# Kernel optimization log

Measured on AMD Instinct MI355X. Metric: run time of the kernel, lower is better.

Reference implementation:

```python
import jax, jax.numpy as jnp
import numpy as np

N = 50000
E = 800000
D_IN = 128
D_HID = 128
NUM_LAYERS = 3


def setup_inputs() -> dict:
    key = jax.random.key(0)
    ks = jax.random.split(key, 8)
    x = jax.random.normal(ks[0], (N, D_IN), dtype=jnp.float32)
    edge_index = jax.random.randint(ks[1], (2, E), 0, N, dtype=jnp.int64)
    edge_weight = jnp.ones((E,), dtype=jnp.float32)
    # GCNConv params: glorot-ish weights [in, out], zero bias
    def w(k, fi, fo):
        return jax.random.normal(k, (fi, fo), dtype=jnp.float32) * (1.0 / np.sqrt(fi))
    W0 = w(ks[2], D_IN, D_HID)
    b0 = jnp.zeros((D_HID,), dtype=jnp.float32)
    W1 = w(ks[3], D_HID, D_HID)
    b1 = jnp.zeros((D_HID,), dtype=jnp.float32)
    W2 = w(ks[4], D_HID, D_HID)
    b2 = jnp.zeros((D_HID,), dtype=jnp.float32)
    return {"x": x, "edge_index": edge_index, "edge_weight": edge_weight,
            "W0": W0, "b0": b0, "W1": W1, "b1": b1, "W2": W2, "b2": b2}


def _gcn_layer(h, src, dst, norm, W, b, n):
    # linear transform then degree-normalized scatter-add aggregation
    h = h @ W                                   # [N, d_out]
    msg = h[src] * norm[:, None]                # gather + scale, [E+N, d_out]
    out = jax.ops.segment_sum(msg, dst, num_segments=n)  # scatter-add
    return out + b


def reference(x, edge_index, edge_weight, W0, b0, W1, b1, W2, b2):
    n = x.shape[0]
    loop = jnp.arange(n, dtype=edge_index.dtype)
    src = jnp.concatenate([edge_index[0], loop])   # add self-loops (fill=1)
    dst = jnp.concatenate([edge_index[1], loop])
    ew = jnp.concatenate([edge_weight, jnp.ones((n,), dtype=edge_weight.dtype)])
    # symmetric normalization: deg computed on target (col), norm = d^-1/2[src]*w*d^-1/2[dst]
    deg = jax.ops.segment_sum(ew, dst, num_segments=n)
    dis = jnp.where(deg > 0, jax.lax.rsqrt(deg), 0.0)
    norm = dis[src] * ew * dis[dst]               # [E+N]
    z = x
    for (W, b) in ((W0, b0), (W1, b1), (W2, b2)):
        z = _gcn_layer(z, src, dst, norm, W, b, n)
        z = jax.nn.relu(z)
    return z
```

## Files before the change

kernel.cpp:

```cpp
#include <hip/hip_runtime.h>

#define D 128
#define NB 250
#define BN 200
#define NBLK 512
#define CAP 7168

typedef float f2v __attribute__((ext_vector_type(2)));
typedef short bf16x8 __attribute__((ext_vector_type(8)));
typedef float f32x4 __attribute__((ext_vector_type(4)));

__device__ __forceinline__ unsigned bf16r(float f) {
  unsigned u = __float_as_uint(f);
  return (u + 0x7fffu + ((u >> 16) & 1u)) >> 16;
}


__global__ __launch_bounds__(256) void k_pre1(const int* __restrict__ dst, int* __restrict__ M, int E,
                                              const float* __restrict__ X, unsigned short* __restrict__ Xb,
                                              int total4, int GC,
                                              const float* __restrict__ W0, const float* __restrict__ W1,
                                              const float* __restrict__ W2, unsigned short* __restrict__ Wt) {
  __shared__ int lh[NB];
  int b = blockIdx.x;
  int tid = threadIdx.x;
  if (b < NBLK) {
    for (int i = tid; i < NB; i += 256) lh[i] = 0;
    __syncthreads();
    const int EPB = (E + NBLK - 1) / NBLK;
    int e0 = b * EPB;
    int e1 = min(e0 + EPB, E);
    for (int e = e0 + tid; e < e1; e += 256) atomicAdd(&lh[dst[e] / BN], 1);
    __syncthreads();
    for (int i = tid; i < NB; i += 256) M[i * NBLK + b] = lh[i];
  } else if (b < NBLK + GC) {
    int i = (b - NBLK) * 256 + tid;
    if (i < total4) {
      float4 v = ((const float4*)X)[i];
      ushort4 o;
      o.x = (unsigned short)bf16r(v.x);
      o.y = (unsigned short)bf16r(v.y);
      o.z = (unsigned short)bf16r(v.z);
      o.w = (unsigned short)bf16r(v.w);
      ((ushort4*)Xb)[i] = o;
    }
  } else {
    int i = (b - NBLK - GC) * 256 + tid;
    if (i < 3 * 16384) {
      int l = i >> 14;
      int r = i & 16383;
      int nn = r >> 7, kk = r & 127;
      const float* W = (l == 0) ? W0 : (l == 1) ? W1 : W2;
      Wt[i] = (unsigned short)bf16r(W[kk * 128 + nn]);
    }
  }
}


__global__ __launch_bounds__(256) void k_blocksum(const int* __restrict__ cnt, int* __restrict__ bsum, int n) {
  int i = blockIdx.x * 256 + threadIdx.x;
  int v = (i < n) ? cnt[i] : 0;
#pragma unroll
  for (int off = 32; off > 0; off >>= 1) v += __shfl_down(v, off);
  __shared__ int ws[4];
  if ((threadIdx.x & 63) == 0) ws[threadIdx.x >> 6] = v;
  __syncthreads();
  if (threadIdx.x == 0) bsum[blockIdx.x] = ws[0] + ws[1] + ws[2] + ws[3];
}

__global__ __launch_bounds__(512) void k_scanb2(const int* __restrict__ bsum, int* __restrict__ boff, int nb) {
  __shared__ int s[512];
  int t = threadIdx.x;
  int v = (t < nb) ? bsum[t] : 0;
  s[t] = v;
  __syncthreads();
#pragma unroll
  for (int off = 1; off < 512; off <<= 1) {
    int u = (t >= off) ? s[t - off] : 0;
    __syncthreads();
    s[t] += u;
    __syncthreads();
  }
  if (t < nb) boff[t] = s[t] - v;
}

__global__ __launch_bounds__(256) void k_scanm(int* __restrict__ M, const int* __restrict__ boff,
                                               int* __restrict__ bbase, int flatN, int Etot) {
  __shared__ int s[256];
  int t = threadIdx.x;
  int i = blockIdx.x * 256 + t;
  int v = (i < flatN) ? M[i] : 0;
  s[t] = v;
  __syncthreads();
#pragma unroll
  for (int off = 1; off < 256; off <<= 1) {
    int u = (t >= off) ? s[t - off] : 0;
    __syncthreads();
    s[t] += u;
    __syncthreads();
  }
  int ex = s[t] - v + boff[blockIdx.x];
  if (i < flatN) {
    M[i] = ex;
    if ((i & (NBLK - 1)) == 0) bbase[i / NBLK] = ex;
  }
  if (i == 0) bbase[NB] = Etot;
}


__global__ __launch_bounds__(256) void k_pre2(const unsigned short* __restrict__ Zb,
                                              const unsigned short* __restrict__ Wt,
                                              unsigned short* __restrict__ H, int n, int GG,
                                              const int* __restrict__ src, const int* __restrict__ dst,
                                              const float* __restrict__ ew, const int* __restrict__ M,
                                              uint2* __restrict__ part, int E) {
  __shared__ int lcur[NB];
  int b = blockIdx.x;
  if (b < GG) {
    int lane = threadIdx.x & 63;
    int wid  = threadIdx.x >> 6;
    int row0 = b * 16;
    int r  = lane & 15;
    int kg = lane >> 4;
    int c0 = wid * 32;
    const size_t abase  = (size_t)(row0 + r) * 128 + kg * 8;
    const size_t b0base = (size_t)(c0 + r) * 128 + kg * 8;
    const size_t b1base = (size_t)(c0 + 16 + r) * 128 + kg * 8;
    f32x4 acc0 = {0.f, 0.f, 0.f, 0.f};
    f32x4 acc1 = {0.f, 0.f, 0.f, 0.f};
#pragma unroll
    for (int k0 = 0; k0 < 128; k0 += 32) {
      bf16x8 a  = *(const bf16x8*)&Zb[abase + k0];
      bf16x8 b0 = *(const bf16x8*)&Wt[b0base + k0];
      bf16x8 b1 = *(const bf16x8*)&Wt[b1base + k0];
      acc0 = __builtin_amdgcn_mfma_f32_16x16x32_bf16(a, b0, acc0, 0, 0, 0);
      acc1 = __builtin_amdgcn_mfma_f32_16x16x32_bf16(a, b1, acc1, 0, 0, 0);
    }
    int orow = row0 + kg * 4;
#pragma unroll
    for (int j = 0; j < 4; ++j) {
      H[(size_t)(orow + j) * 128 + c0 + r]      = (unsigned short)bf16r(acc0[j]);
      H[(size_t)(orow + j) * 128 + c0 + 16 + r] = (unsigned short)bf16r(acc1[j]);
    }
  } else {
    int blk = b - GG;
    int tid = threadIdx.x;
    for (int i = tid; i < NB; i += 256) lcur[i] = M[i * NBLK + blk];
    __syncthreads();
    const int EPB = (E + NBLK - 1) / NBLK;
    int e0 = blk * EPB;
    int e1 = min(e0 + EPB, E);
    for (int e = e0 + tid; e < e1; e += 256) {
      int d = dst[e];
      int bkt = d / BN;
      int dlow = d - bkt * BN;
      int p = atomicAdd(&lcur[bkt], 1);
      uint2 rec;
      rec.x = (unsigned)src[e] | ((unsigned)dlow << 24);
      rec.y = __float_as_uint(ew[e]);
      part[p] = rec;
    }
  }
}


__global__ __launch_bounds__(256) void k_bsort(const uint2* __restrict__ part, const int* __restrict__ bbase,
                                               uint2* __restrict__ csr, int* __restrict__ rowptr,
                                               float* __restrict__ dis, int n, int E) {
  __shared__ uint2 stage[CAP];
  __shared__ int lh[BN];
  __shared__ float ldeg[BN];
  __shared__ int s[256];
  int b = blockIdx.x;
  int tid = threadIdx.x;
  int base = bbase[b];
  int cnt = bbase[b + 1] - base;
  for (int i = tid; i < BN; i += 256) { lh[i] = 0; ldeg[i] = 0.f; }
  __syncthreads();
  for (int i = tid; i < cnt; i += 256) {
    uint2 r = part[base + i];
    if (i < CAP) stage[i] = r;
    int dlow = r.x >> 24;
    atomicAdd(&lh[dlow], 1);
    atomicAdd(&ldeg[dlow], __uint_as_float(r.y));
  }
  __syncthreads();
  int v = (tid < BN) ? lh[tid] : 0;
  s[tid] = v;
  __syncthreads();
#pragma unroll
  for (int off = 1; off < 256; off <<= 1) {
    int u = (tid >= off) ? s[tid - off] : 0;
    __syncthreads();
    s[tid] += u;
    __syncthreads();
  }
  int ex = s[tid] - v;
  if (tid < BN) {
    lh[tid] = ex;
    int node = b * BN + tid;
    rowptr[node] = base + ex;
    dis[node] = rsqrtf(1.0f + ldeg[tid]);
  }
  if (b == 0 && tid == 0) rowptr[n] = E;
  __syncthreads();
  for (int i = tid; i < cnt; i += 256) {
    uint2 r = (i < CAP) ? stage[i] : part[base + i];
    int dlow = r.x >> 24;
    int p = atomicAdd(&lh[dlow], 1);
    uint2 o;
    o.x = r.x & 0x00FFFFFFu;
    o.y = r.y;
    csr[base + p] = o;
  }
}


__global__ __launch_bounds__(256) void k_gemm(const unsigned short* __restrict__ Zb,
                                              const unsigned short* __restrict__ Wt,
                                              unsigned short* __restrict__ H, int n) {
  int lane = threadIdx.x & 63;
  int wid  = threadIdx.x >> 6;
  int row0 = blockIdx.x * 16;
  int r  = lane & 15;
  int kg = lane >> 4;
  int c0 = wid * 32;
  const size_t abase  = (size_t)(row0 + r) * 128 + kg * 8;
  const size_t b0base = (size_t)(c0 + r) * 128 + kg * 8;
  const size_t b1base = (size_t)(c0 + 16 + r) * 128 + kg * 8;
  f32x4 acc0 = {0.f, 0.f, 0.f, 0.f};
  f32x4 acc1 = {0.f, 0.f, 0.f, 0.f};
#pragma unroll
  for (int k0 = 0; k0 < 128; k0 += 32) {
    bf16x8 a  = *(const bf16x8*)&Zb[abase + k0];
    bf16x8 b0 = *(const bf16x8*)&Wt[b0base + k0];
    bf16x8 b1 = *(const bf16x8*)&Wt[b1base + k0];
    acc0 = __builtin_amdgcn_mfma_f32_16x16x32_bf16(a, b0, acc0, 0, 0, 0);
    acc1 = __builtin_amdgcn_mfma_f32_16x16x32_bf16(a, b1, acc1, 0, 0, 0);
  }
  int orow = row0 + kg * 4;
#pragma unroll
  for (int j = 0; j < 4; ++j) {
    H[(size_t)(orow + j) * 128 + c0 + r]      = (unsigned short)bf16r(acc0[j]);
    H[(size_t)(orow + j) * 128 + c0 + 16 + r] = (unsigned short)bf16r(acc1[j]);
  }
}


__global__ __launch_bounds__(256) void k_agg(const unsigned* __restrict__ Hb, const int* __restrict__ rowptr,
                                             const f2v* __restrict__ csr, const float* __restrict__ dis,
                                             const float* __restrict__ bias, unsigned* __restrict__ outb,
                                             float* __restrict__ outf, int n) {
  int node = __builtin_amdgcn_readfirstlane(blockIdx.x * 4 + (threadIdx.x >> 6));
  if (node >= n) return;
  int lane = threadIdx.x & 63;
  float ax = 0.f, ay = 0.f;
  int e = rowptr[node];
  const int end = rowptr[node + 1];
  for (; e + 4 <= end; e += 4) {
    f2v r0 = __builtin_nontemporal_load(&csr[e]);
    f2v r1 = __builtin_nontemporal_load(&csr[e + 1]);
    f2v r2 = __builtin_nontemporal_load(&csr[e + 2]);
    f2v r3 = __builtin_nontemporal_load(&csr[e + 3]);
    int s0 = __float_as_int(r0.x);
    int s1 = __float_as_int(r1.x);
    int s2 = __float_as_int(r2.x);
    int s3 = __float_as_int(r3.x);
    float w0 = r0.y * dis[s0];
    float w1 = r1.y * dis[s1];
    float w2 = r2.y * dis[s2];
    float w3 = r3.y * dis[s3];
    unsigned g0 = Hb[(size_t)s0 * 64 + lane];
    unsigned g1 = Hb[(size_t)s1 * 64 + lane];
    unsigned g2 = Hb[(size_t)s2 * 64 + lane];
    unsigned g3 = Hb[(size_t)s3 * 64 + lane];
    ax = fmaf(__uint_as_float(g0 << 16), w0, ax); ay = fmaf(__uint_as_float(g0 & 0xffff0000u), w0, ay);
    ax = fmaf(__uint_as_float(g1 << 16), w1, ax); ay = fmaf(__uint_as_float(g1 & 0xffff0000u), w1, ay);
    ax = fmaf(__uint_as_float(g2 << 16), w2, ax); ay = fmaf(__uint_as_float(g2 & 0xffff0000u), w2, ay);
    ax = fmaf(__uint_as_float(g3 << 16), w3, ax); ay = fmaf(__uint_as_float(g3 & 0xffff0000u), w3, ay);
  }
  for (; e < end; ++e) {
    f2v r0 = __builtin_nontemporal_load(&csr[e]);
    int s0 = __float_as_int(r0.x);
    float w0 = r0.y * dis[s0];
    unsigned g0 = Hb[(size_t)s0 * 64 + lane];
    ax = fmaf(__uint_as_float(g0 << 16), w0, ax); ay = fmaf(__uint_as_float(g0 & 0xffff0000u), w0, ay);
  }
  float dn = dis[node];
  float sn = dn * dn;
  unsigned hv = Hb[(size_t)node * 64 + lane];
  float hvx = __uint_as_float(hv << 16);
  float hvy = __uint_as_float(hv & 0xffff0000u);
  float2 bv = ((const float2*)bias)[lane];
  float ox = fmaxf(fmaf(dn, ax, fmaf(sn, hvx, bv.x)), 0.f);
  float oy = fmaxf(fmaf(dn, ay, fmaf(sn, hvy, bv.y)), 0.f);
  if (outb) {
    outb[(size_t)node * 64 + lane] = bf16r(ox) | (bf16r(oy) << 16);
  } else {
    f2v o; o.x = ox; o.y = oy;
    __builtin_nontemporal_store(o, (f2v*)outf + (size_t)node * 64 + lane);
  }
}


extern "C" void kernel_launch(void* const* d_in, const int* in_sizes, int n_in,
                              void* d_out, int out_size, void* d_ws, size_t ws_size,
                              hipStream_t stream) {
  const float* x  = (const float*)d_in[0];
  const int*   ei = (const int*)d_in[1];
  const float* ew = (const float*)d_in[2];
  const float* W0 = (const float*)d_in[3];
  const float* W1 = (const float*)d_in[5];
  const float* W2 = (const float*)d_in[7];
  const float* bl[3] = {(const float*)d_in[4], (const float*)d_in[6], (const float*)d_in[8]};

  const int n = in_sizes[0] / D;
  const int E = in_sizes[1] / 2;
  const int* src = ei;
  const int* dst = ei + E;

  char* p = (char*)d_ws;
  unsigned short* Zb     = (unsigned short*)p; p += (size_t)n * D * 2;
  unsigned short* H      = (unsigned short*)p; p += (size_t)n * D * 2;
  float*          dis    = (float*)p;          p += (size_t)n * 4;
  int*            rowptr = (int*)p;            p += (size_t)(n + 1) * 4;
  int*            M      = (int*)p;            p += (size_t)NB * NBLK * 4;
  int*            bbase  = (int*)p;            p += (size_t)(NB + 1) * 4;
  int*            bsum2  = (int*)p;            p += 512 * 4;
  int*            boff2  = (int*)p;            p += 512 * 4;
  uint2*          part   = (uint2*)p;          p += (size_t)E * 8;
  uint2*          csr    = (uint2*)p;          p += (size_t)E * 8;
  unsigned short* Wt     = (unsigned short*)p; p += 3 * 16384 * 2;
  (void)ws_size; (void)n_in;

  const int total4 = n * D / 4;
  const int GC = (total4 + 255) / 256;
  const int GW = (3 * 16384 + 255) / 256;
  const int GG = n / 16;
  const int flatN = NB * NBLK;
  const int GS = flatN / 256;

  k_pre1<<<NBLK + GC + GW, 256, 0, stream>>>(dst, M, E, x, Zb, total4, GC, W0, W1, W2, Wt);
  k_blocksum<<<GS, 256, 0, stream>>>(M, bsum2, flatN);
  k_scanb2<<<1, 512, 0, stream>>>(bsum2, boff2, GS);
  k_scanm<<<GS, 256, 0, stream>>>(M, boff2, bbase, flatN, E);
  k_pre2<<<GG + NBLK, 256, 0, stream>>>(Zb, Wt, H, n, GG, src, dst, ew, M, part, E);
  k_bsort<<<NB, 256, 0, stream>>>(part, bbase, csr, rowptr, dis, n, E);

  float* outp = (float*)d_out;
  k_agg<<<(n + 3) / 4, 256, 0, stream>>>((const unsigned*)H, rowptr, (const f2v*)csr, dis, bl[0], (unsigned*)Zb, outp, n);
  for (int l = 1; l < 3; ++l) {
    k_gemm<<<GG, 256, 0, stream>>>(Zb, Wt + l * 16384, H, n);
    unsigned* ob = (l == 2) ? nullptr : (unsigned*)Zb;
    k_agg<<<(n + 3) / 4, 256, 0, stream>>>((const unsigned*)H, rowptr, (const f2v*)csr, dis, bl[l], ob, outp, n);
  }
}
```

Before: 213.9 us.

## Pack CSR edges into 4-byte records with prescaled bf16 weights and padded rows

Each CSR edge shrinks from 8 bytes to 4: a 16-bit source index plus a bf16 weight already multiplied by dis[src]. This removes the random dis gather and halves edge-stream traffic in all three aggregation passes. Rows are padded to multiples of four with zero entries so the aggregation loop uses one vector load per four edges and needs no tail loop. Degree computation moves into a separate k_deg kernel so dis exists before the CSR is built. The cost is an extra launch, reduced weight precision, and a 16-bit source index that only holds while the node count stays below 65536.

After: 244.7 us. 14.4% more time.

```diff
diff --git a/kernel.cpp b/kernel.cpp
--- a/kernel.cpp
+++ b/kernel.cpp
@@ -5,6 +5,7 @@
 #define BN 200
 #define NBLK 512
 #define CAP 7168
+#define PADB 600
 
 typedef float f2v __attribute__((ext_vector_type(2)));
 typedef short bf16x8 __attribute__((ext_vector_type(8)));
@@ -164,29 +165,47 @@
 }
 
 
+__global__ __launch_bounds__(256) void k_deg(const uint2* __restrict__ part, const int* __restrict__ bbase,
+                                             float* __restrict__ dis, int n) {
+  __shared__ float ldeg[BN];
+  int b = blockIdx.x;
+  int tid = threadIdx.x;
+  int base = bbase[b];
+  int cnt = bbase[b + 1] - base;
+  for (int i = tid; i < BN; i += 256) ldeg[i] = 0.f;
+  __syncthreads();
+  for (int i = tid; i < cnt; i += 256) {
+    uint2 r = part[base + i];
+    atomicAdd(&ldeg[r.x >> 24], __uint_as_float(r.y));
+  }
+  __syncthreads();
+  for (int t = tid; t < BN; t += 256) dis[b * BN + t] = rsqrtf(1.0f + ldeg[t]);
+}
+
+
 __global__ __launch_bounds__(256) void k_bsort(const uint2* __restrict__ part, const int* __restrict__ bbase,
-                                               uint2* __restrict__ csr, int* __restrict__ rowptr,
-                                               float* __restrict__ dis, int n, int E) {
+                                               const float* __restrict__ dis, unsigned* __restrict__ csr4,
+                                               int* __restrict__ rowptr, int n, int Etot) {
   __shared__ uint2 stage[CAP];
   __shared__ int lh[BN];
-  __shared__ float ldeg[BN];
   __shared__ int s[256];
   int b = blockIdx.x;
   int tid = threadIdx.x;
   int base = bbase[b];
   int cnt = bbase[b + 1] - base;
-  for (int i = tid; i < BN; i += 256) { lh[i] = 0; ldeg[i] = 0.f; }
+  int R  = ((base + 3) & ~3) + b * PADB;
+  int Rn = ((bbase[b + 1] + 3) & ~3) + (b + 1) * PADB;
+  for (int i = tid; i < BN; i += 256) lh[i] = 0;
   __syncthreads();
   for (int i = tid; i < cnt; i += 256) {
     uint2 r = part[base + i];
     if (i < CAP) stage[i] = r;
-    int dlow = r.x >> 24;
-    atomicAdd(&lh[dlow], 1);
-    atomicAdd(&ldeg[dlow], __uint_as_float(r.y));
-  }
-  __syncthreads();
-  int v = (tid < BN) ? lh[tid] : 0;
-  s[tid] = v;
+    atomicAdd(&lh[r.x >> 24], 1);
+  }
+  __syncthreads();
+  int c = (tid < BN) ? lh[tid] : 0;
+  int pc = (c + 3) & ~3;
+  s[tid] = pc;
   __syncthreads();
 #pragma unroll
   for (int off = 1; off < 256; off <<= 1) {
@@ -195,23 +214,23 @@
     s[tid] += u;
     __syncthreads();
   }
-  int ex = s[tid] - v;
+  int ex = s[tid] - pc;
   if (tid < BN) {
     lh[tid] = ex;
-    int node = b * BN + tid;
-    rowptr[node] = base + ex;
-    dis[node] = rsqrtf(1.0f + ldeg[tid]);
-  }
-  if (b == 0 && tid == 0) rowptr[n] = E;
+    rowptr[b * BN + tid] = R + ex;
+  }
+  if (b == 0 && tid == 0) rowptr[n] = ((Etot + 3) & ~3) + NB * PADB;
+  __syncthreads();
+  int len = Rn - R;
+  for (int i = tid; i < len; i += 256) csr4[R + i] = 0u;
   __syncthreads();
   for (int i = tid; i < cnt; i += 256) {
     uint2 r = (i < CAP) ? stage[i] : part[base + i];
     int dlow = r.x >> 24;
+    unsigned srcv = r.x & 0x00FFFFFFu;
+    float w = __uint_as_float(r.y) * dis[srcv];
     int p = atomicAdd(&lh[dlow], 1);
-    uint2 o;
-    o.x = r.x & 0x00FFFFFFu;
-    o.y = r.y;
-    csr[base + p] = o;
+    csr4[R + p] = srcv | (bf16r(w) << 16);
   }
 }
 
@@ -248,7 +267,7 @@
 
 
 __global__ __launch_bounds__(256) void k_agg(const unsigned* __restrict__ Hb, const int* __restrict__ rowptr,
-                                             const f2v* __restrict__ csr, const float* __restrict__ dis,
+                                             const unsigned* __restrict__ csr4, const float* __restrict__ dis,
                                              const float* __restrict__ bias, unsigned* __restrict__ outb,
                                              float* __restrict__ outf, int n) {
   int node = __builtin_amdgcn_readfirstlane(blockIdx.x * 4 + (threadIdx.x >> 6));
@@ -257,19 +276,12 @@
   float ax = 0.f, ay = 0.f;
   int e = rowptr[node];
   const int end = rowptr[node + 1];
-  for (; e + 4 <= end; e += 4) {
-    f2v r0 = __builtin_nontemporal_load(&csr[e]);
-    f2v r1 = __builtin_nontemporal_load(&csr[e + 1]);
-    f2v r2 = __builtin_nontemporal_load(&csr[e + 2]);
-    f2v r3 = __builtin_nontemporal_load(&csr[e + 3]);
-    int s0 = __float_as_int(r0.x);
-    int s1 = __float_as_int(r1.x);
-    int s2 = __float_as_int(r2.x);
-    int s3 = __float_as_int(r3.x);
-    float w0 = r0.y * dis[s0];
-    float w1 = r1.y * dis[s1];
-    float w2 = r2.y * dis[s2];
-    float w3 = r3.y * dis[s3];
+  for (; e < end; e += 4) {
+    uint4 rq = *(const uint4*)&csr4[e];
+    int s0 = rq.x & 0xFFFFu; float w0 = __uint_as_float(rq.x & 0xFFFF0000u);
+    int s1 = rq.y & 0xFFFFu; float w1 = __uint_as_float(rq.y & 0xFFFF0000u);
+    int s2 = rq.z & 0xFFFFu; float w2 = __uint_as_float(rq.z & 0xFFFF0000u);
+    int s3 = rq.w & 0xFFFFu; float w3 = __uint_as_float(rq.w & 0xFFFF0000u);
     unsigned g0 = Hb[(size_t)s0 * 64 + lane];
     unsigned g1 = Hb[(size_t)s1 * 64 + lane];
     unsigned g2 = Hb[(size_t)s2 * 64 + lane];
@@ -278,13 +290,6 @@
     ax = fmaf(__uint_as_float(g1 << 16), w1, ax); ay = fmaf(__uint_as_float(g1 & 0xffff0000u), w1, ay);
     ax = fmaf(__uint_as_float(g2 << 16), w2, ax); ay = fmaf(__uint_as_float(g2 & 0xffff0000u), w2, ay);
     ax = fmaf(__uint_as_float(g3 << 16), w3, ax); ay = fmaf(__uint_as_float(g3 & 0xffff0000u), w3, ay);
-  }
-  for (; e < end; ++e) {
-    f2v r0 = __builtin_nontemporal_load(&csr[e]);
-    int s0 = __float_as_int(r0.x);
-    float w0 = r0.y * dis[s0];
-    unsigned g0 = Hb[(size_t)s0 * 64 + lane];
-    ax = fmaf(__uint_as_float(g0 << 16), w0, ax); ay = fmaf(__uint_as_float(g0 & 0xffff0000u), w0, ay);
   }
   float dn = dis[node];
   float sn = dn * dn;
@@ -329,7 +334,7 @@
   int*            bsum2  = (int*)p;            p += 512 * 4;
   int*            boff2  = (int*)p;            p += 512 * 4;
   uint2*          part   = (uint2*)p;          p += (size_t)E * 8;
-  uint2*          csr    = (uint2*)p;          p += (size_t)E * 8;
+  unsigned*       csr4   = (unsigned*)p;       p += ((size_t)E + NB * PADB + 64) * 4;
   unsigned short* Wt     = (unsigned short*)p; p += 3 * 16384 * 2;
   (void)ws_size; (void)n_in;
 
@@ -345,13 +350,14 @@
   k_scanb2<<<1, 512, 0, stream>>>(bsum2, boff2, GS);
   k_scanm<<<GS, 256, 0, stream>>>(M, boff2, bbase, flatN, E);
   k_pre2<<<GG + NBLK, 256, 0, stream>>>(Zb, Wt, H, n, GG, src, dst, ew, M, part, E);
-  k_bsort<<<NB, 256, 0, stream>>>(part, bbase, csr, rowptr, dis, n, E);
+  k_deg<<<NB, 256, 0, stream>>>(part, bbase, dis, n);
+  k_bsort<<<NB, 256, 0, stream>>>(part, bbase, dis, csr4, rowptr, n, E);
 
   float* outp = (float*)d_out;
-  k_agg<<<(n + 3) / 4, 256, 0, stream>>>((const unsigned*)H, rowptr, (const f2v*)csr, dis, bl[0], (unsigned*)Zb, outp, n);
+  k_agg<<<(n + 3) / 4, 256, 0, stream>>>((const unsigned*)H, rowptr, csr4, dis, bl[0], (unsigned*)Zb, outp, n);
   for (int l = 1; l < 3; ++l) {
     k_gemm<<<GG, 256, 0, stream>>>(Zb, Wt + l * 16384, H, n);
     unsigned* ob = (l == 2) ? nullptr : (unsigned*)Zb;
-    k_agg<<<(n + 3) / 4, 256, 0, stream>>>((const unsigned*)H, rowptr, (const f2v*)csr, dis, bl[l], ob, outp, n);
-  }
-}
+    k_agg<<<(n + 3) / 4, 256, 0, stream>>>((const unsigned*)H, rowptr, csr4, dis, bl[l], ob, outp, n);
+  }
+}
```
